# Kernel optimization log

Measured on AMD Instinct MI355X. Metric: run time of the kernel, lower is better.

Reference implementation:

```python
import jax, jax.numpy as jnp
import numpy as np

N, E = 32768, 262144
IN_C, OUT_C = 128, 128
N_GRAPHS = 64


def setup_inputs() -> dict:
    key = jax.random.key(0)
    ks = jax.random.split(key, 8)
    x = jax.random.normal(ks[0], (N, IN_C), dtype=jnp.float32)
    edge_index = jax.random.randint(ks[1], (2, E), 0, N, dtype=jnp.int32)
    batch = jnp.sort(jax.random.randint(ks[2], (N,), 0, N_GRAPHS, dtype=jnp.int32))
    rand = jax.random.uniform(ks[3], (E,), dtype=jnp.float32)  # replaces random.random() draws
    lim_t = 1.0 / np.sqrt(IN_C)
    W_t = jax.random.uniform(ks[4], (IN_C, OUT_C), jnp.float32, -lim_t, lim_t)
    b_t = jax.random.uniform(ks[5], (OUT_C,), jnp.float32, -lim_t, lim_t)
    lim_s = 1.0 / np.sqrt(OUT_C)
    W_s = jax.random.uniform(ks[6], (OUT_C, 1), jnp.float32, -lim_s, lim_s)
    b_s = jax.random.uniform(ks[7], (1,), jnp.float32, -lim_s, lim_s)
    return dict(x=x, edge_index=edge_index, batch=batch, rand=rand,
                W_t=W_t, b_t=b_t, W_s=W_s, b_s=b_s)


def _greedy_match(scores, src, dst, rand, n):
    """Sequential greedy edge matching over score-sorted edges.
    Returns (order, cid_sorted, n_merged): cid_sorted[i] is the cluster id
    assigned to sorted edge i, or -1 if rejected/skipped."""
    scores = jax.lax.stop_gradient(scores)  # indices are non-differentiable (torch uses .item())
    rand = jax.lax.stop_gradient(rand)
    order = jnp.argsort(-scores)
    s_o, d_o = src[order], dst[order]
    acc = rand[order] <= scores[order]  # torch: skip edge if r > edge_score

    def step(carry, inp):
        avail, nxt = carry
        s, t, a = inp
        ok = a & avail[s] & avail[t]
        cid = jnp.where(ok, nxt, -1)
        avail = avail.at[s].set(avail[s] & ~ok)
        avail = avail.at[t].set(avail[t] & ~ok)
        return (avail, nxt + ok.astype(jnp.int32)), cid

    (_, n_merged), cid_sorted = jax.lax.scan(
        step, (jnp.ones((n,), bool), jnp.int32(0)), (s_o, d_o, acc))
    return order, cid_sorted, n_merged


def reference(x, edge_index, batch, rand, W_t, b_t, W_s, b_s):
    n = x.shape[0]
    src, dst = edge_index[0], edge_index[1]
    # merge_edge_sum + transform (eval mode, dropout p=0)
    x_merged = (x[src] + x[dst]) @ W_t + b_t          # [E, OUT_C]
    x_self = (x + x) @ W_t + b_t                      # [N, OUT_C] (self-edge merge)
    e = jax.nn.sigmoid((x_merged @ W_s).reshape(-1) + b_s[0])  # [E] edge scores

    order, cid_sorted, n_merged = _greedy_match(e, src, dst, rand, n)
    ok = cid_sorted >= 0                              # accepted sorted edges
    s_o, d_o = src[order], dst[order]

    # node -> cluster assignment (sentinel index n is dropped)
    cluster = jnp.full((n,), -1, jnp.int32)
    cluster = cluster.at[jnp.where(ok, s_o, n)].set(cid_sorted, mode='drop')
    cluster = cluster.at[jnp.where(ok, d_o, n)].set(cid_sorted, mode='drop')
    remaining = cluster < 0
    rem_rank = jnp.cumsum(remaining.astype(jnp.int32)) - 1  # ascending node order, like set iteration
    cluster = jnp.where(remaining, n_merged + rem_rank, cluster)
    num_clusters = n_merged + remaining.sum().astype(jnp.int32)

    # pooled features, padded to [n, OUT_C]; rows [0, num_clusters) are valid
    mcid = jnp.where(ok, cid_sorted, n)
    new_x = jnp.zeros((n, x_merged.shape[1]), x.dtype)
    new_x = new_x.at[mcid].set(x_merged[order], mode='drop')
    new_x = new_x.at[jnp.where(remaining, cluster, n)].set(x_self, mode='drop')

    # per-cluster edge score (1.0 for unmerged singleton nodes)
    new_edge_score = jnp.ones((n,), e.dtype).at[mcid].set(e[order], mode='drop')

    # new batch vector: new_batch[cluster[v]] = batch[v]
    new_batch = jnp.zeros((n,), batch.dtype).at[cluster].set(batch)

    # remapped edges + coalesce/remove_self_loops expressed as a validity mask
    new_ei = cluster[edge_index]                      # [2, E]
    key = new_ei[0].astype(jnp.int64) * n + new_ei[1].astype(jnp.int64)
    perm = jnp.argsort(key)
    ksorted = key[perm]
    first = jnp.concatenate([jnp.array([True]), ksorted[1:] != ksorted[:-1]])
    unique = jnp.zeros((key.shape[0],), bool).at[perm].set(first)
    edge_valid = unique & (new_ei[0] != new_ei[1])

    return new_x, cluster, new_batch, new_edge_score, num_clusters, new_ei, edge_valid, e
```

## Files before the change

### kernel.cpp

```cpp
#include <hip/hip_runtime.h>
#include <stdint.h>

typedef unsigned int u32;
typedef unsigned long long u64;

#define NN 32768
#define NE 262144
#define NC 128

#define O0 0u
#define O1 4194304u
#define O2 4227072u
#define O3 4259840u
#define O4 4292608u
#define O5 4292609u
#define O6 4816897u
#define O7 5079041u

#define HCAP (1u<<19)
#define NFULL 8
#define CNT0 8
#define MCAP 16384
#define SCAP 32768
#define SNB 32
#define MAXK 0xFFFFFFFFFFFFFFFFull
#define EMASK 0x3FFFFu

__global__ void ep_init(const float* Wt, const float* Ws, const float* bt, const float* bs,
                        double* u, double* c0, u32* counters,
                        u64* b0, u64* b1, u32* avail, int* cl,
                        u32* tkey, u32* tmin, unsigned char* premat, u32* mflag) {
    u32 i = blockIdx.x*blockDim.x + threadIdx.x;
    if (blockIdx.x == 0 && threadIdx.x < 128) {
        int r = threadIdx.x;
        double s = 0.0;
        for (int j = 0; j < NC; j++) s += (double)Wt[r*NC+j] * (double)Ws[j];
        u[r] = s;
        if (r == 0) {
            double c = 0.0;
            for (int j = 0; j < NC; j++) c += (double)bt[j] * (double)Ws[j];
            *c0 = c + (double)bs[0];
        }
    }
    if (i < 64) counters[i] = 0u;
    if (i < NN) { b0[i] = MAXK; b1[i] = MAXK; cl[i] = -1; }
    if (i < NN/32) avail[i] = 0xFFFFFFFFu;
    if (i < SCAP) mflag[i] = 0u;
    ((unsigned short*)premat)[i] = 0;
    for (u32 j = i; j < HCAP; j += 131072u) { tkey[j] = 0xFFFFFFFFu; tmin[j] = 0xFFFFFFFFu; }
}

__global__ void ep_ynode(const float* x, const double* u, double* y) {
    int gid = blockIdx.x*blockDim.x + threadIdx.x;
    int v = gid >> 6, lane = threadIdx.x & 63;
    if (v >= NN) return;
    double t = (double)x[v*NC+lane]*u[lane] + (double)x[v*NC+lane+64]*u[lane+64];
    for (int off = 32; off; off >>= 1) t += __shfl_down(t, off, 64);
    if (lane == 0) y[v] = t;
}

__global__ void ep_escore(const int* src, const int* dst, const float* rnd, const double* y,
                          const double* c0, u64* fkey, u32* counters, float* out) {
    int e = blockIdx.x*blockDim.x + threadIdx.x;
    if (e >= NE) return;
    int s = src[e], d = dst[e];
    double z = y[s] + y[d] + *c0;
    double sc = 1.0/(1.0 + exp(-z));
    out[O7 + e] = (float)sc;
    u64 b = (u64)__double_as_longlong(z);
    u64 ord = (b & 0x8000000000000000ull) ? ~b : (b | 0x8000000000000000ull);
    u64 P = ((~ord) & 0xFFFFFFFFFFFC0000ull) | (u64)(u32)e;
    if ((double)rnd[e] <= sc) {
        u32 p = atomicAdd(&counters[CNT0], 1u);
        fkey[p] = P;
    }
}

__device__ __forceinline__ bool ep_bit(const u32* a, u32 v) { return (a[v>>5] >> (v&31)) & 1u; }

__global__ void ep_rA(const u64* fkey, const int* src, const int* dst,
                      const u32* cnt, u64* bt, const u32* avail) {
    u32 n = *cnt;
    for (u32 i = blockIdx.x*blockDim.x + threadIdx.x; i < n; i += 65536u) {
        u64 P = fkey[i];
        u32 e = (u32)(P & EMASK);
        u32 s = (u32)src[e], d = (u32)dst[e];
        if (ep_bit(avail, s) && ep_bit(avail, d)) {
            atomicMin(&bt[s], P); atomicMin(&bt[d], P);
        }
    }
}

__global__ void ep_rB(const u64* fkey, const int* src, const int* dst,
                      const u32* cnt, u32* cntN, u64* fkeyN,
                      const u64* bt, u64* btN, u32* avail,
                      u64* mkey, unsigned char* premat, u32* counters) {
    u32 n = *cnt;
    for (u32 i = blockIdx.x*blockDim.x + threadIdx.x; i < n; i += 65536u) {
        u64 P = fkey[i];
        u32 e = (u32)(P & EMASK);
        u32 s = (u32)src[e], d = (u32)dst[e];
        if (!ep_bit(avail, s) || !ep_bit(avail, d)) continue;
        if (bt[s] == P && bt[d] == P) {
            u32 slot = atomicAdd(&counters[2], 1u);
            mkey[slot] = P;
            premat[e] = 1;
            atomicAnd(&avail[s>>5], ~(1u<<(s&31)));
            atomicAnd(&avail[d>>5], ~(1u<<(d&31)));
        } else {
            u32 p = atomicAdd(cntN, 1u);
            fkeyN[p] = P;
            btN[s] = MAXK; btN[d] = MAXK;
        }
    }
}

__global__ void ep_merge(const u64* mk, const u64* fk, u32* counters, u64* ck) {
    u32 i = blockIdx.x*blockDim.x + threadIdx.x;
    u32 nm0 = counters[2];
    u32 cr  = counters[CNT0+NFULL];
    if (i == 0) { u32 tot = nm0 + cr; counters[4] = tot > SCAP ? SCAP : tot; }
    u64 K = MAXK;
    if (i < nm0) K = mk[i];
    else if (i < nm0 + cr && i < SCAP) K = fk[i-nm0];
    ck[i] = K;
}

__device__ __forceinline__ u64 ep_peers(u32 d, bool real) {
    u64 m = ~0ull;
    #pragma unroll
    for (int b = 0; b < 8; b++) {
        u64 bb = __ballot((d >> b) & 1u);
        m &= ((d >> b) & 1u) ? bb : ~bb;
    }
    return m & __ballot(real);
}

__device__ __forceinline__ void ms_gbar(u32* bar) {
    __syncthreads();
    if (threadIdx.x == 0) {
        __threadfence();
        u32 gen = atomicAdd(&bar[1], 0u);
        if (atomicAdd(&bar[0], 1u) == SNB - 1) {
            atomicExch(&bar[0], 0u);
            __threadfence();
            atomicAdd(&bar[1], 1u);
        } else {
            while (atomicAdd(&bar[1], 0u) == gen) __builtin_amdgcn_s_sleep(8);
        }
        __threadfence();
    }
    __syncthreads();
}

__global__ void __launch_bounds__(64) ms_sort(u64* a, u64* b, u32* hist,
                                              const u32* counters, u32* bar) {
    __shared__ u32 h[256];
    int t = threadIdx.x;
    u32 blk = blockIdx.x;
    u32 total = counters[4];
    u64 *ki = a, *ko = b;
    for (int p = 0; p < 6; p++) {
        int shift = 16 + p*8;
        h[t] = 0; h[t+64] = 0; h[t+128] = 0; h[t+192] = 0;
        for (int j = 0; j < 16; j++) {
            u32 idx = blk*1024u + (u32)j*64u + (u32)t;
            bool real = idx < total;
            u64 k = real ? ki[idx] : MAXK;
            u32 d = (u32)(k >> shift) & 255u;
            u64 m = ep_peers(d, real);
            if (real && t == (__ffsll((unsigned long long)m) - 1)) h[d] += (u32)__popcll(m);
        }
        hist[(u32)t*SNB + blk]       = h[t];
        hist[((u32)t+64)*SNB + blk]  = h[t+64];
        hist[((u32)t+128)*SNB + blk] = h[t+128];
        hist[((u32)t+192)*SNB + blk] = h[t+192];
        ms_gbar(bar);
        if (blk == 0) {
            int b2 = t*128;
            u32 s = 0;
            for (int j = 0; j < 128; j++) s += hist[b2+j];
            u32 x = s;
            for (int off = 1; off < 64; off <<= 1) { u32 yv = __shfl_up(x, off, 64); if (t >= off) x += yv; }
            u32 run = x - s;
            for (int j = 0; j < 128; j++) { u32 tmp = hist[b2+j]; hist[b2+j] = run; run += tmp; }
        }
        ms_gbar(bar);
        h[t] = 0; h[t+64] = 0; h[t+128] = 0; h[t+192] = 0;
        for (int j = 0; j < 16; j++) {
            u32 idx = blk*1024u + (u32)j*64u + (u32)t;
            bool real = idx < total;
            u64 k = real ? ki[idx] : MAXK;
            u32 d = (u32)(k >> shift) & 255u;
            u64 m = ep_peers(d, real);
            if (real) {
                u32 rank = (u32)__popcll(m & (((u64)1 << t) - 1ull));
                int leader = __ffsll((unsigned long long)m) - 1;
                u32 base = 0;
                if (t == leader) { base = h[d]; h[d] = base + (u32)__popcll(m); }
                base = __shfl(base, leader, 64);
                ko[hist[d*SNB + blk] + base + rank] = k;
            }
        }
        ms_gbar(bar);
        u64* tp = ki; ki = ko; ko = tp;
    }
}

__global__ void __launch_bounds__(1024) ep_walk(const u64* sk, const int* src, const int* dst,
                                                const unsigned char* premat, u32* counters,
                                                const u32* availG, u32* mflag, u32* msums) {
    __shared__ u32 avail[1024];
    __shared__ u32 claim[16384];
    __shared__ u32 part[1024];
    __shared__ u32 segs[32];
    int t = threadIdx.x;
    avail[t] = availG[t];
    for (int j = t; j < 16384; j += 1024) claim[j] = 0xFFFFFFFFu;
    __syncthreads();
    u32 total = counters[4];
    u32 iterTag = 0x3FFFFFu;
    for (u32 base = 0; base < total; base += 1024) {
        u32 i = base + (u32)t;
        bool have = i < total;
        u32 s = 0, d = 0;
        int st = 1;
        if (have) {
            u32 e = (u32)(sk[i] & EMASK);
            if (premat[e]) {
                mflag[i] = 1u;
            } else {
                s = (u32)src[e]; d = (u32)dst[e];
                if (((avail[s>>5]>>(s&31))&1u) && ((avail[d>>5]>>(d&31))&1u)) st = 0;
            }
        }
        u32 hs = s & 16383u, hd = d & 16383u;
        for (int guard = 0; guard < 4096; guard++) {
            u32 tag = (iterTag << 10) | (u32)t;
            if (st == 0) { atomicMin(&claim[hs], tag); atomicMin(&claim[hd], tag); }
            __syncthreads();
            if (st == 0) {
                bool aok = ((avail[s>>5]>>(s&31))&1u) && ((avail[d>>5]>>(d&31))&1u);
                if (!aok) st = 1;
                else if (claim[hs] == tag && claim[hd] == tag) {
                    st = 2;
                    atomicAnd(&avail[s>>5], ~(1u<<(s&31)));
                    atomicAnd(&avail[d>>5], ~(1u<<(d&31)));
                    mflag[i] = 1u;
                }
            }
            iterTag--;
            if (__syncthreads_count(st == 0) == 0) break;
        }
    }
    __threadfence_block();
    __syncthreads();
    u32 p = 0; int b2 = t*32;
    for (int j = 0; j < 32; j++) p += mflag[b2+j];
    part[t] = p;
    __syncthreads();
    if (t < 32) { u32 sg = 0; for (int j = 0; j < 32; j++) sg += part[t*32+j]; segs[t] = sg; }
    __syncthreads();
    if (t == 0) { u32 a = 0; for (int g = 0; g < 32; g++) { msums[g] = a; a += segs[g]; } counters[2] = a; }
}

__global__ void ep_memit(const u64* sk, const int* src, const int* dst,
                         const u32* mflag, const u32* msums,
                         const int* batch, u64* Mlist, int* cl, float* out) {
    __shared__ u32 w[16];
    int t = threadIdx.x;
    u32 i = blockIdx.x*1024 + t;
    u32 m = mflag[i];
    u32 x = m;
    for (int off = 1; off < 64; off <<= 1) { u32 y = __shfl_up(x, off, 64); if ((t&63) >= off) x += y; }
    if ((t&63) == 63) w[t>>6] = x;
    __syncthreads();
    if (t < 16) {
        u32 ww = w[t];
        for (int off = 1; off < 16; off <<= 1) { u32 y = __shfl_up(ww, off, 16); if (t >= off) ww += y; }
        w[t] = ww;
    }
    __syncthreads();
    u32 excl = ((t>>6) ? w[(t>>6)-1] : 0u) + x - m;
    if (m) {
        u32 cid = msums[blockIdx.x] + excl;
        u32 e = (u32)(sk[i] & EMASK);
        u32 s = (u32)src[e], d = (u32)dst[e];
        Mlist[cid] = ((u64)e << 30) | ((u64)s << 15) | (u64)d;
        cl[s] = (int)cid; cl[d] = (int)cid;
        u32 mx = s > d ? s : d;
        out[O2 + cid] = (float)batch[mx];
        out[O3 + cid] = out[O7 + e];
    }
}

__global__ void ep_scanN(int* cl, u32* counters, u32* slist, float* out) {
    __shared__ u32 w[16];
    int t = threadIdx.x;
    int base = t*32;
    u32 s = 0;
    for (int j = 0; j < 32; j++) s += (cl[base+j] < 0) ? 1u : 0u;
    u32 x = s;
    for (int off = 1; off < 64; off <<= 1) { u32 y = __shfl_up(x, off, 64); if ((t&63) >= off) x += y; }
    if ((t&63) == 63) w[t>>6] = x;
    __syncthreads();
    if (t < 16) {
        u32 ww = w[t];
        for (int off = 1; off < 16; off <<= 1) { u32 y = __shfl_up(ww, off, 16); if (t >= off) ww += y; }
        w[t] = ww;
    }
    __syncthreads();
    u32 excl = ((t>>6) ? w[(t>>6)-1] : 0u) + x - s;
    u32 total = w[15];
    u32 nm = counters[2];
    if (t == 0) {
        counters[3] = nm + total;
        counters[6] = total;
        out[O4] = (float)(nm + total);
    }
    u32 run = nm + excl;
    for (int j = 0; j < 32; j++) {
        if (cl[base+j] < 0) {
            slist[run - nm] = (u32)(base + j);
            cl[base+j] = (int)(run++);
        }
    }
}

__global__ void ep_out_nodes(const int* cl, const int* batch, const u32* counters, float* out) {
    int v = blockIdx.x*blockDim.x + threadIdx.x;
    if (v >= NN) return;
    u32 nm = counters[2], ncl = counters[3];
    int c = cl[v];
    out[O1 + v] = (float)c;
    if (c >= (int)nm) out[O2 + c] = (float)batch[v];
    if (v >= (int)nm) out[O3 + v] = 1.0f;
    if (v >= (int)ncl) out[O2 + v] = 0.0f;
}

__global__ void ep_newx_m(const float* x, const float* Wt, const float* bt,
                          const u64* Mlist, const u32* counters, float* out) {
    __shared__ u64 ml[32];
    __shared__ float m[32][128];
    u32 nm = counters[2];
    u32 base = blockIdx.x * 32u;
    if (base >= nm) return;
    int t = threadIdx.x, lane = t & 63, wv = t >> 6;
    if (t < 32) { u32 r = base + (u32)t; ml[t] = (r < nm) ? Mlist[r] : 0ull; }
    __syncthreads();
    for (int i = t; i < 4096; i += 256) {
        int r = i >> 7, k = i & 127;
        u64 v = ml[r];
        u32 s = (u32)((v>>15)&0x7FFF), d = (u32)(v&0x7FFF);
        m[r][k] = x[s*NC+k] + x[d*NC+k];
    }
    __syncthreads();
    float a0[8], a1[8];
    #pragma unroll
    for (int r = 0; r < 8; r++) { a0[r] = bt[lane]; a1[r] = bt[lane+64]; }
    for (int k = 0; k < 128; k++) {
        float w0 = Wt[k*NC+lane], w1 = Wt[k*NC+lane+64];
        #pragma unroll
        for (int r = 0; r < 8; r++) { float mm = m[wv*8+r][k]; a0[r] += mm*w0; a1[r] += mm*w1; }
    }
    #pragma unroll
    for (int r = 0; r < 8; r++) {
        u32 row = base + (u32)(wv*8 + r);
        if (row < nm) {
            out[O0 + (size_t)row*NC + lane]      = a0[r];
            out[O0 + (size_t)row*NC + lane + 64] = a1[r];
        }
    }
}

__global__ void ep_newx_s(const float* x, const float* Wt, const float* bt,
                          const u32* slist, const u32* counters, float* out) {
    __shared__ u32 nodes[32];
    __shared__ float m[32][128];
    u32 nm = counters[2], ncl = counters[3], sc = counters[6];
    u32 base = nm + blockIdx.x * 32u;
    if (base >= NN) return;
    int t = threadIdx.x, lane = t & 63, wv = t >> 6;
    if (base >= ncl) {
        for (int i = t; i < 4096; i += 256) {
            u32 row = base + (u32)(i >> 7);
            if (row < NN) out[O0 + (size_t)row*NC + (i & 127)] = 0.0f;
        }
        return;
    }
    if (t < 32) { u32 p = base - nm + (u32)t; nodes[t] = (p < sc) ? slist[p] : slist[0]; }
    __syncthreads();
    for (int i = t; i < 4096; i += 256) {
        int r = i >> 7, k = i & 127;
        m[r][k] = 2.0f * x[nodes[r]*NC + k];
    }
    __syncthreads();
    float a0[8], a1[8];
    #pragma unroll
    for (int r = 0; r < 8; r++) { a0[r] = bt[lane]; a1[r] = bt[lane+64]; }
    for (int k = 0; k < 128; k++) {
        float w0 = Wt[k*NC+lane], w1 = Wt[k*NC+lane+64];
        #pragma unroll
        for (int r = 0; r < 8; r++) { float mm = m[wv*8+r][k]; a0[r] += mm*w0; a1[r] += mm*w1; }
    }
    #pragma unroll
    for (int r = 0; r < 8; r++) {
        u32 row = base + (u32)(wv*8 + r);
        if (row >= NN) continue;
        if (row < ncl) {
            out[O0 + (size_t)row*NC + lane]      = a0[r];
            out[O0 + (size_t)row*NC + lane + 64] = a1[r];
        } else {
            out[O0 + (size_t)row*NC + lane]      = 0.0f;
            out[O0 + (size_t)row*NC + lane + 64] = 0.0f;
        }
    }
}

__global__ void ep_newei(const int* src, const int* dst, const int* cl,
                         u32* tkey, u32* tmin, u32* eslot, float* out) {
    int e = blockIdx.x*blockDim.x + threadIdx.x;
    if (e >= NE) return;
    u32 cs = (u32)cl[src[e]], cd = (u32)cl[dst[e]];
    out[O5 + e]      = (float)cs;
    out[O5 + NE + e] = (float)cd;
    u32 key = (cs << 15) | cd;
    u32 slot = ((key * 2654435761u) >> 11) & (HCAP-1);
    while (true) {
        u32 k = tkey[slot];
        if (k == key) break;
        if (k == 0xFFFFFFFFu) {
            u32 old = atomicCAS(&tkey[slot], 0xFFFFFFFFu, key);
            if (old == 0xFFFFFFFFu || old == key) break;
        }
        slot = (slot + 1) & (HCAP-1);
    }
    eslot[e] = slot | ((cs != cd) ? 0x80000000u : 0u);
    atomicMin(&tmin[slot], (u32)e);
}

__global__ void ep_valid(const u32* tmin, const u32* eslot, float* out) {
    int e = blockIdx.x*blockDim.x + threadIdx.x;
    if (e >= NE) return;
    u32 sl = eslot[e];
    bool valid = (tmin[sl & 0x7FFFFFFFu] == (u32)e) && (sl >> 31);
    out[O6 + e] = valid ? 1.0f : 0.0f;
}

extern "C" void kernel_launch(void* const* d_in, const int* in_sizes, int n_in,
                              void* d_out, int out_size, void* d_ws, size_t ws_size,
                              hipStream_t stream) {
    (void)in_sizes; (void)n_in; (void)out_size; (void)ws_size;
    const float* x    = (const float*)d_in[0];
    const int*   ei   = (const int*)d_in[1];
    const int*   src  = ei;
    const int*   dst  = ei + NE;
    const int*   batch= (const int*)d_in[2];
    const float* rnd  = (const float*)d_in[3];
    const float* Wt   = (const float*)d_in[4];
    const float* bt   = (const float*)d_in[5];
    const float* Ws   = (const float*)d_in[6];
    const float* bs   = (const float*)d_in[7];
    float* out = (float*)d_out;

    char* w = (char*)d_ws;
    double* u  = (double*)w;
    double* c0 = (double*)(w + 1024);
    u32* counters = (u32*)(w + 2048);
    size_t off = 4096;
    double* y   = (double*)(w + off); off += (size_t)NN*8;
    u64* fkeyA  = (u64*)(w + off); off += (size_t)NE*8;
    u64* fkeyB  = (u64*)(w + off); off += (size_t)NE*8;
    u64* mkeyA  = (u64*)(w + off); off += (size_t)MCAP*8;
    u64* combK  = (u64*)(w + off); off += (size_t)SCAP*8;
    u64* combK2 = (u64*)(w + off); off += (size_t)SCAP*8;
    u64* bt0    = (u64*)(w + off); off += (size_t)NN*8;
    u64* bt1    = (u64*)(w + off); off += (size_t)NN*8;
    u32* avail  = (u32*)(w + off); off += NN/8;
    int* cl     = (int*)(w + off); off += (size_t)NN*4;
    u64* Mlist  = (u64*)(w + off); off += (size_t)NN*8;
    u32* hist   = (u32*)(w + off); off += 8192*4;
    u32* mflag  = (u32*)(w + off); off += (size_t)SCAP*4;
    u32* msums  = (u32*)(w + off); off += 64*4;
    u32* slist  = (u32*)(w + off); off += (size_t)NN*4;
    unsigned char* premat = (unsigned char*)(w + off); off += NE;
    u32* tkey   = (u32*)(w + off); off += (size_t)HCAP*4;
    u32* tmin   = (u32*)(w + off); off += (size_t)HCAP*4;
    u32* eslot  = (u32*)(w + off); off += (size_t)NE*4;

    ep_init<<<512, 256, 0, stream>>>(Wt, Ws, bt, bs, u, c0, counters,
                                     bt0, bt1, avail, cl, tkey, tmin, premat, mflag);
    ep_ynode<<<8192, 256, 0, stream>>>(x, u, y);
    ep_escore<<<1024, 256, 0, stream>>>(src, dst, rnd, y, c0, fkeyA, counters, out);

    u64 *fk = fkeyA, *fk2 = fkeyB;
    u64 *bc = bt0, *bn = bt1;
    for (u32 rd = 0; rd < NFULL; rd++) {
        ep_rA<<<256, 256, 0, stream>>>(fk, src, dst, &counters[CNT0+rd], bc, avail);
        ep_rB<<<256, 256, 0, stream>>>(fk, src, dst, &counters[CNT0+rd], &counters[CNT0+rd+1],
                                       fk2, bc, bn, avail, mkeyA, premat, counters);
        u64* tp;
        tp = fk; fk = fk2; fk2 = tp;
        tp = bc; bc = bn; bn = tp;
    }

    ep_merge<<<SNB, 1024, 0, stream>>>(mkeyA, fk, counters, combK);
    ms_sort<<<SNB, 64, 0, stream>>>(combK, combK2, hist, counters, &counters[32]);

    ep_walk<<<1, 1024, 0, stream>>>(combK, src, dst, premat, counters, avail, mflag, msums);
    ep_memit<<<SNB, 1024, 0, stream>>>(combK, src, dst, mflag, msums, batch, Mlist, cl, out);

    ep_scanN<<<1, 1024, 0, stream>>>(cl, counters, slist, out);
    ep_out_nodes<<<128, 256, 0, stream>>>(cl, batch, counters, out);

    ep_newx_m<<<512, 256, 0, stream>>>(x, Wt, bt, Mlist, counters, out);
    ep_newx_s<<<1024, 256, 0, stream>>>(x, Wt, bt, slist, counters, out);

    ep_newei<<<1024, 256, 0, stream>>>(src, dst, cl, tkey, tmin, eslot, out);
    ep_valid<<<1024, 256, 0, stream>>>(tmin, eslot, out);
}
```

Measured before the change: 772.9 us.

## Replace grid-barrier radix sort with per-pass histogram, scan and scatter kernels

The persistent 32-block radix sort that synchronised its passes with atomic spin barriers becomes three separate kernel launches per pass (histogram, scan, scatter), so kernel boundaries provide the ordering. The prefix scan now runs in a 256-thread block instead of a single wavefront of block 0. This removes spin-wait barrier overhead but adds 18 kernel launches in place of one. Six passes is an even count, so the result still lands in combK.

```diff
diff --git a/kernel.cpp b/kernel.cpp
--- a/kernel.cpp
+++ b/kernel.cpp
@@ -136,74 +136,62 @@
     return m & __ballot(real);
 }
 
-__device__ __forceinline__ void ms_gbar(u32* bar) {
-    __syncthreads();
-    if (threadIdx.x == 0) {
-        __threadfence();
-        u32 gen = atomicAdd(&bar[1], 0u);
-        if (atomicAdd(&bar[0], 1u) == SNB - 1) {
-            atomicExch(&bar[0], 0u);
-            __threadfence();
-            atomicAdd(&bar[1], 1u);
-        } else {
-            while (atomicAdd(&bar[1], 0u) == gen) __builtin_amdgcn_s_sleep(8);
-        }
-        __threadfence();
-    }
-    __syncthreads();
-}
-
-__global__ void __launch_bounds__(64) ms_sort(u64* a, u64* b, u32* hist,
-                                              const u32* counters, u32* bar) {
+__global__ void ms_hist(const u64* key, u32* hist, int shift, const u32* counters) {
     __shared__ u32 h[256];
     int t = threadIdx.x;
+    u32 total = counters[4];
+    h[t] = 0; h[t+64] = 0; h[t+128] = 0; h[t+192] = 0;
     u32 blk = blockIdx.x;
+    for (int j = 0; j < 16; j++) {
+        u32 idx = blk*1024u + (u32)j*64u + (u32)t;
+        bool real = idx < total;
+        u64 k = real ? key[idx] : MAXK;
+        u32 d = (u32)(k >> shift) & 255u;
+        u64 m = ep_peers(d, real);
+        if (real && t == (__ffsll((unsigned long long)m) - 1)) h[d] += (u32)__popcll(m);
+    }
+    hist[(u32)t*SNB + blk]       = h[t];
+    hist[((u32)t+64)*SNB + blk]  = h[t+64];
+    hist[((u32)t+128)*SNB + blk] = h[t+128];
+    hist[((u32)t+192)*SNB + blk] = h[t+192];
+}
+
+__global__ void ms_scan(u32* hist) {
+    __shared__ u32 w[4];
+    int t = threadIdx.x;
+    int base = t*32;
+    u32 s = 0;
+    for (int j = 0; j < 32; j++) s += hist[base+j];
+    u32 x = s;
+    for (int off = 1; off < 64; off <<= 1) { u32 yv = __shfl_up(x, off, 64); if ((t&63) >= off) x += yv; }
+    if ((t&63) == 63) w[t>>6] = x;
+    __syncthreads();
+    if (t == 0) { u32 a = 0; for (int k = 0; k < 4; k++) { u32 tmp = w[k]; w[k] = a; a += tmp; } }
+    __syncthreads();
+    u32 run = w[t>>6] + x - s;
+    for (int j = 0; j < 32; j++) { u32 tmp = hist[base+j]; hist[base+j] = run; run += tmp; }
+}
+
+__global__ void ms_scat(const u64* ki, u64* ko, const u32* hist, int shift, const u32* counters) {
+    __shared__ u32 cnt[256];
+    int t = threadIdx.x;
     u32 total = counters[4];
-    u64 *ki = a, *ko = b;
-    for (int p = 0; p < 6; p++) {
-        int shift = 16 + p*8;
-        h[t] = 0; h[t+64] = 0; h[t+128] = 0; h[t+192] = 0;
-        for (int j = 0; j < 16; j++) {
-            u32 idx = blk*1024u + (u32)j*64u + (u32)t;
-            bool real = idx < total;
-            u64 k = real ? ki[idx] : MAXK;
-            u32 d = (u32)(k >> shift) & 255u;
-            u64 m = ep_peers(d, real);
-            if (real && t == (__ffsll((unsigned long long)m) - 1)) h[d] += (u32)__popcll(m);
-        }
-        hist[(u32)t*SNB + blk]       = h[t];
-        hist[((u32)t+64)*SNB + blk]  = h[t+64];
-        hist[((u32)t+128)*SNB + blk] = h[t+128];
-        hist[((u32)t+192)*SNB + blk] = h[t+192];
-        ms_gbar(bar);
-        if (blk == 0) {
-            int b2 = t*128;
-            u32 s = 0;
-            for (int j = 0; j < 128; j++) s += hist[b2+j];
-            u32 x = s;
-            for (int off = 1; off < 64; off <<= 1) { u32 yv = __shfl_up(x, off, 64); if (t >= off) x += yv; }
-            u32 run = x - s;
-            for (int j = 0; j < 128; j++) { u32 tmp = hist[b2+j]; hist[b2+j] = run; run += tmp; }
-        }
-        ms_gbar(bar);
-        h[t] = 0; h[t+64] = 0; h[t+128] = 0; h[t+192] = 0;
-        for (int j = 0; j < 16; j++) {
-            u32 idx = blk*1024u + (u32)j*64u + (u32)t;
-            bool real = idx < total;
-            u64 k = real ? ki[idx] : MAXK;
-            u32 d = (u32)(k >> shift) & 255u;
-            u64 m = ep_peers(d, real);
-            if (real) {
-                u32 rank = (u32)__popcll(m & (((u64)1 << t) - 1ull));
-                int leader = __ffsll((unsigned long long)m) - 1;
-                u32 base = 0;
-                if (t == leader) { base = h[d]; h[d] = base + (u32)__popcll(m); }
-                base = __shfl(base, leader, 64);
-                ko[hist[d*SNB + blk] + base + rank] = k;
-            }
-        }
-        ms_gbar(bar);
-        u64* tp = ki; ki = ko; ko = tp;
+    cnt[t] = 0; cnt[t+64] = 0; cnt[t+128] = 0; cnt[t+192] = 0;
+    u32 blk = blockIdx.x;
+    for (int j = 0; j < 16; j++) {
+        u32 idx = blk*1024u + (u32)j*64u + (u32)t;
+        bool real = idx < total;
+        u64 k = real ? ki[idx] : MAXK;
+        u32 d = (u32)(k >> shift) & 255u;
+        u64 m = ep_peers(d, real);
+        if (real) {
+            u32 rank = (u32)__popcll(m & (((u64)1 << t) - 1ull));
+            int leader = __ffsll((unsigned long long)m) - 1;
+            u32 base = 0;
+            if (t == leader) { base = cnt[d]; cnt[d] = base + (u32)__popcll(m); }
+            base = __shfl(base, leader, 64);
+            ko[hist[d*SNB + blk] + base + rank] = k;
+        }
     }
 }
 
@@ -505,7 +493,14 @@
     }
 
     ep_merge<<<SNB, 1024, 0, stream>>>(mkeyA, fk, counters, combK);
-    ms_sort<<<SNB, 64, 0, stream>>>(combK, combK2, hist, counters, &counters[32]);
+    u64 *ki = combK, *ko = combK2;
+    for (int p = 0; p < 6; p++) {
+        int shift = 16 + p*8;
+        ms_hist<<<SNB, 64, 0, stream>>>(ki, hist, shift, counters);
+        ms_scan<<<1, 256, 0, stream>>>(hist);
+        ms_scat<<<SNB, 64, 0, stream>>>(ki, ko, hist, shift, counters);
+        u64* tp = ki; ki = ko; ko = tp;
+    }
 
     ep_walk<<<1, 1024, 0, stream>>>(combK, src, dst, premat, counters, avail, mflag, msums);
     ep_memit<<<SNB, 1024, 0, stream>>>(combK, src, dst, mflag, msums, batch, Mlist, cl, out);
```

Result: faster. 720.8 us (-6.7%).
